# Kernel optimization log

Measured on AMD Instinct MI355X. Metric: run time of the kernel, lower is better.

## Reference

```python
import jax, jax.numpy as jnp
import numpy as np

N_NODES = 100000
N_EDGES = 1600000
IN_DIM = 128
HID_DIM = 128
OUT_DIM = 2


def sage_conv(x, src, dst, deg_inv, W_l, W_r, b):
    # mean-aggregate neighbor features: messages flow src -> dst
    agg = jax.ops.segment_sum(x[src], dst, num_segments=N_NODES)  # [N, d_in]
    agg = agg * deg_inv[:, None]
    # PyG SAGEConv: out = lin_l(aggr) + lin_r(x); bias only on lin_l
    return agg @ W_l + x @ W_r + b


def setup_inputs() -> dict:
    key = jax.random.key(0)
    ks = jax.random.split(key, 9)
    x = jax.random.normal(ks[0], (N_NODES, IN_DIM), dtype=jnp.float32)
    edge_index = jax.random.randint(ks[1], (2, N_EDGES), 0, N_NODES, dtype=jnp.int64)

    def glorot(k, shape):
        lim = float(np.sqrt(6.0 / (shape[0] + shape[1])))
        return jax.random.uniform(k, shape, jnp.float32, -lim, lim)

    return {
        "x": x,
        "edge_index": edge_index,
        "W1_l": glorot(ks[2], (IN_DIM, HID_DIM)),
        "W1_r": glorot(ks[3], (IN_DIM, HID_DIM)),
        "b1": jnp.zeros((HID_DIM,), jnp.float32),
        "W2_l": glorot(ks[4], (HID_DIM, HID_DIM)),
        "W2_r": glorot(ks[5], (HID_DIM, HID_DIM)),
        "b2": jnp.zeros((HID_DIM,), jnp.float32),
        "W3_l": glorot(ks[6], (HID_DIM, OUT_DIM)),
        "W3_r": glorot(ks[7], (HID_DIM, OUT_DIM)),
        "b3": jnp.zeros((OUT_DIM,), jnp.float32),
    }


def reference(x, edge_index, W1_l, W1_r, b1, W2_l, W2_r, b2, W3_l, W3_r, b3):
    src, dst = edge_index[0], edge_index[1]
    # mean-aggregation normalization: 1/in-degree (clamped to >=1)
    deg = jax.ops.segment_sum(jnp.ones((N_EDGES,), jnp.float32), dst, num_segments=N_NODES)
    deg_inv = 1.0 / jnp.maximum(deg, 1.0)

    h = sage_conv(x, src, dst, deg_inv, W1_l, W1_r, b1)
    h = jax.nn.relu(h)  # dropout is identity in eval mode
    h = sage_conv(h, src, dst, deg_inv, W2_l, W2_r, b2)
    h = jax.nn.relu(h)
    h = sage_conv(h, src, dst, deg_inv, W3_l, W3_r, b3)
    h = jax.nn.relu(h)
    return jax.nn.log_softmax(h, axis=1)
```

## Files before the change

kernel.cpp:

```cpp
#include <hip/hip_runtime.h>
#include <hip/hip_bf16.h>
#include <math.h>

#define DIM 128

typedef __attribute__((ext_vector_type(8))) short bf16x8;
typedef __attribute__((ext_vector_type(4))) float f32x4;

__device__ __forceinline__ ushort f2bf(float f) {
  unsigned u = __float_as_uint(f);
  return (ushort)((u + 0x7FFFu + ((u >> 16) & 1u)) >> 16);
}
__device__ __forceinline__ float bf2f(ushort h) {
  return __uint_as_float(((unsigned)h) << 16);
}

__global__ __launch_bounds__(256) void prep_kernel(
    const int* __restrict__ dst, unsigned* __restrict__ deg, unsigned* __restrict__ rank, int E,
    const float* __restrict__ x, ushort* __restrict__ xh, long total,
    const float* __restrict__ W1l, const float* __restrict__ W1r,
    const float* __restrict__ W2l, const float* __restrict__ W2r,
    ushort* __restrict__ tabs, int H, int C) {
  const int bid = blockIdx.x;
  const int r = bid % 3;
  const int q = bid / 3;
  if (r == 0) {
    if (q < H) {
      int gid = q * 256 + threadIdx.x;
      if (gid < E) rank[gid] = atomicAdd(&deg[dst[gid]], 1u);
    }
    return;
  }
  int id2 = q * 2 + (r - 1);
  if (id2 < C) {
    long i = ((long)id2 * 256 + threadIdx.x) * 4;
    if (i >= total) return;
    float4 v = *(const float4*)(x + i);
    uint2 Hh;
    Hh.x = (unsigned)f2bf(v.x) | ((unsigned)f2bf(v.y) << 16);
    Hh.y = (unsigned)f2bf(v.z) | ((unsigned)f2bf(v.w) << 16);
    *(uint2*)(xh + i) = Hh;
    return;
  }
  id2 -= C;
  if (id2 >= 256) return;
  int m = id2 >> 6;
  const float* W = (m == 0) ? W1l : (m == 1) ? W1r : (m == 2) ? W2l : W2r;
  ushort* Ht = tabs + (size_t)m * 16384;
  int idx = (id2 & 63) * 256 + threadIdx.x;
  int k = idx >> 7, n = idx & 127;
  Ht[n * DIM + k] = f2bf(W[idx]);
}

__global__ __launch_bounds__(256) void scan_block_kernel(const unsigned* __restrict__ deg,
                                                         unsigned* __restrict__ excl,
                                                         unsigned* __restrict__ partial,
                                                         float* __restrict__ dinv, int N) {
  __shared__ unsigned s[256];
  int i = blockIdx.x * 256 + threadIdx.x;
  unsigned v = (i < N) ? deg[i] : 0u;
  if (i < N) dinv[i] = 1.0f / fmaxf((float)v, 1.0f);
  s[threadIdx.x] = v;
  __syncthreads();
#pragma unroll
  for (int d = 1; d < 256; d <<= 1) {
    unsigned t = (threadIdx.x >= d) ? s[threadIdx.x - d] : 0u;
    __syncthreads();
    s[threadIdx.x] += t;
    __syncthreads();
  }
  if (i < N) excl[i] = s[threadIdx.x] - v;
  if (threadIdx.x == 255) partial[blockIdx.x] = s[255];
}

__global__ __launch_bounds__(256) void scan_partials_kernel(unsigned* __restrict__ partial, int B) {
  __shared__ unsigned s[256];
  __shared__ unsigned carry;
  if (threadIdx.x == 0) carry = 0u;
  __syncthreads();
  for (int base = 0; base < B; base += 256) {
    int i = base + threadIdx.x;
    unsigned v = (i < B) ? partial[i] : 0u;
    s[threadIdx.x] = v;
    __syncthreads();
#pragma unroll
    for (int d = 1; d < 256; d <<= 1) {
      unsigned t = (threadIdx.x >= d) ? s[threadIdx.x - d] : 0u;
      __syncthreads();
      s[threadIdx.x] += t;
      __syncthreads();
    }
    if (i < B) partial[i] = carry + s[threadIdx.x] - v;
    __syncthreads();
    if (threadIdx.x == 0) carry += s[255];
    __syncthreads();
  }
}

__global__ __launch_bounds__(256) void add_offsets_kernel(const unsigned* __restrict__ excl,
                                                          const unsigned* __restrict__ partial,
                                                          unsigned* __restrict__ off, int N, int E) {
  int i = blockIdx.x * 256 + threadIdx.x;
  if (i < N) off[i] = excl[i] + partial[i >> 8];
  if (i == N) off[N] = (unsigned)E;
}

__global__ __launch_bounds__(256) void csr_fill_kernel(const int* __restrict__ src,
                                                       const int* __restrict__ dst,
                                                       const unsigned* __restrict__ rank,
                                                       const unsigned* __restrict__ off,
                                                       int* __restrict__ csr_src, int E) {
  int e = blockIdx.x * 256 + threadIdx.x;
  if (e >= E) return;
  csr_src[off[dst[e]] + rank[e]] = src[e];
}

__global__ __launch_bounds__(256) void gather_wave_kernel(
    const ushort* __restrict__ featH, const int* __restrict__ csr_src,
    const unsigned* __restrict__ off, const float* __restrict__ dinv,
    ushort* __restrict__ aggH, int N) {
  const int node = (blockIdx.x * 256 + threadIdx.x) >> 6;
  if (node >= N) return;
  const int lane = threadIdx.x & 63;
  const int eslot = lane >> 4;
  const int col = lane & 15;
  const unsigned beg = off[node], end = off[node + 1];
  const ushort* fbase = featH + col * 8;

  float acc[8];
#pragma unroll
  for (int t = 0; t < 8; ++t) acc[t] = 0.f;

  auto accum = [&](int4 v) {
    unsigned w0 = (unsigned)v.x, w1 = (unsigned)v.y, w2 = (unsigned)v.z, w3 = (unsigned)v.w;
    acc[0] += __uint_as_float(w0 << 16);
    acc[1] += __uint_as_float(w0 & 0xFFFF0000u);
    acc[2] += __uint_as_float(w1 << 16);
    acc[3] += __uint_as_float(w1 & 0xFFFF0000u);
    acc[4] += __uint_as_float(w2 << 16);
    acc[5] += __uint_as_float(w2 & 0xFFFF0000u);
    acc[6] += __uint_as_float(w3 << 16);
    acc[7] += __uint_as_float(w3 & 0xFFFF0000u);
  };

  unsigned base = beg;
  for (; base + 16 <= end; base += 16) {
    int s0 = csr_src[base + eslot];
    int s1 = csr_src[base + 4 + eslot];
    int s2 = csr_src[base + 8 + eslot];
    int s3 = csr_src[base + 12 + eslot];
    int4 v0 = *(const int4*)(fbase + (size_t)s0 * DIM);
    int4 v1 = *(const int4*)(fbase + (size_t)s1 * DIM);
    int4 v2 = *(const int4*)(fbase + (size_t)s2 * DIM);
    int4 v3 = *(const int4*)(fbase + (size_t)s3 * DIM);
    accum(v0); accum(v1); accum(v2); accum(v3);
  }
  for (; base + 8 <= end; base += 8) {
    int s0 = csr_src[base + eslot];
    int s1 = csr_src[base + 4 + eslot];
    int4 v0 = *(const int4*)(fbase + (size_t)s0 * DIM);
    int4 v1 = *(const int4*)(fbase + (size_t)s1 * DIM);
    accum(v0); accum(v1);
  }
  for (unsigned e = base + eslot; e < end; e += 4) {
    int s = csr_src[e];
    int4 v = *(const int4*)(fbase + (size_t)s * DIM);
    accum(v);
  }

#pragma unroll
  for (int t = 0; t < 8; ++t) {
    acc[t] += __shfl_xor(acc[t], 32, 64);
    acc[t] += __shfl_xor(acc[t], 16, 64);
  }

  if (eslot == 0) {
    float di = dinv[node];
    unsigned ph[4];
#pragma unroll
    for (int t = 0; t < 4; ++t) {
      ph[t] = (unsigned)f2bf(acc[2 * t] * di) | ((unsigned)f2bf(acc[2 * t + 1] * di) << 16);
    }
    *(int4*)(aggH + (size_t)node * DIM + col * 8) =
        make_int4((int)ph[0], (int)ph[1], (int)ph[2], (int)ph[3]);
  }
}

__global__ __launch_bounds__(256) void sage_mfma_kernel(
    const ushort* __restrict__ aggH, const ushort* xH,
    const ushort* __restrict__ WlH, const ushort* __restrict__ WrH,
    const float* __restrict__ bias,
    const float* __restrict__ W3l, const float* __restrict__ W3r,
    ushort* __restrict__ outH, float* __restrict__ y, int N) {
  __shared__ ushort As[128 * 64];
  __shared__ ushort Bs[128 * 64];

  const int tid = threadIdx.x;
  const int bm = blockIdx.x * 128;
  const int wave = tid >> 6;
  const int lane = tid & 63;
  const int l15 = lane & 15;
  const int quad = lane >> 4;
  const int wm = wave >> 1;
  const int wn = wave & 1;

  f32x4 acc[4][4];
#pragma unroll
  for (int i = 0; i < 4; ++i)
#pragma unroll
    for (int j = 0; j < 4; ++j) acc[i][j] = (f32x4){0.f, 0.f, 0.f, 0.f};

  for (int g = 0; g < 4; ++g) {
    const ushort* Ap = (g < 2) ? aggH : xH;
    const ushort* Wp = (g < 2) ? WlH : WrH;
    const int kt = (g & 1) << 6;
    __syncthreads();
#pragma unroll
    for (int c = 0; c < 4; ++c) {
      int flat = c * 256 + tid;
      int row = flat >> 3;
      int kg = flat & 7;
      int swz = (kg ^ (row & 7)) << 3;
      int grow = bm + row;
      if (grow >= N) grow = N - 1;
      *(int4*)(&As[row * 64 + swz]) = *(const int4*)(Ap + (size_t)grow * DIM + kt + kg * 8);
      *(int4*)(&Bs[row * 64 + swz]) = *(const int4*)(Wp + (size_t)row * DIM + kt + kg * 8);
    }
    __syncthreads();
#pragma unroll
    for (int ks = 0; ks < 2; ++ks) {
      bf16x8 af[4], bfr[4];
      int kg = (ks << 2) + quad;
#pragma unroll
      for (int i = 0; i < 4; ++i) {
        int ar = (wm << 6) + (i << 4) + l15;
        af[i] = *(const bf16x8*)(&As[ar * 64 + ((kg ^ (ar & 7)) << 3)]);
        int br = (wn << 6) + (i << 4) + l15;
        bfr[i] = *(const bf16x8*)(&Bs[br * 64 + ((kg ^ (br & 7)) << 3)]);
      }
#pragma unroll
      for (int i = 0; i < 4; ++i)
#pragma unroll
        for (int j = 0; j < 4; ++j)
          acc[i][j] = __builtin_amdgcn_mfma_f32_16x16x32_bf16(af[i], bfr[j], acc[i][j], 0, 0, 0);
    }
  }

  __syncthreads();
  float* WcF = reinterpret_cast<float*>(As);
  float* YpF = reinterpret_cast<float*>(As) + 512;

  if (W3l) {
    for (int t = tid; t < 512; t += 256) {
      int col = t >> 2, c = t & 3;
      WcF[t] = (c < 2) ? W3l[col * 2 + c] : W3r[col * 2 + (c - 2)];
    }
    __syncthreads();
  }

  float bv[4];
#pragma unroll
  for (int j = 0; j < 4; ++j) bv[j] = bias[(wn << 6) + (j << 4) + l15];

#pragma unroll
  for (int i = 0; i < 4; ++i) {
#pragma unroll
    for (int r = 0; r < 4; ++r) {
      const int rowl = (wm << 6) + (i << 4) + (quad << 2) + r;
      const int grow = bm + rowl;
      float p0 = 0.f, p1 = 0.f, p2 = 0.f, p3 = 0.f;
#pragma unroll
      for (int j = 0; j < 4; ++j) {
        int col = (wn << 6) + (j << 4) + l15;
        float v = fmaxf(acc[i][j][r] + bv[j], 0.f);
        ushort h = f2bf(v);
        if (outH && grow < N) outH[(size_t)grow * DIM + col] = h;
        if (W3l) {
          float qv = bf2f(h);
          p0 += qv * WcF[col * 4 + 0];
          p1 += qv * WcF[col * 4 + 1];
          p2 += qv * WcF[col * 4 + 2];
          p3 += qv * WcF[col * 4 + 3];
        }
      }
      if (W3l) {
#pragma unroll
        for (int o = 1; o < 16; o <<= 1) {
          p0 += __shfl_xor(p0, o, 64);
          p1 += __shfl_xor(p1, o, 64);
          p2 += __shfl_xor(p2, o, 64);
          p3 += __shfl_xor(p3, o, 64);
        }
        if (l15 == 0) {
          YpF[(rowl * 4 + 0) * 2 + wn] = p0;
          YpF[(rowl * 4 + 1) * 2 + wn] = p1;
          YpF[(rowl * 4 + 2) * 2 + wn] = p2;
          YpF[(rowl * 4 + 3) * 2 + wn] = p3;
        }
      }
    }
  }

  if (W3l) {
    __syncthreads();
    for (int t = tid; t < 512; t += 256) {
      int grow = bm + (t >> 2);
      if (grow < N) y[(size_t)grow * 4 + (t & 3)] = YpF[t * 2 + 0] + YpF[t * 2 + 1];
    }
  }
}

__global__ __launch_bounds__(256) void final3_kernel(const float* __restrict__ y,
                                                     const int* __restrict__ csr_src,
                                                     const unsigned* __restrict__ off,
                                                     const float* __restrict__ dinv,
                                                     const float* __restrict__ b3,
                                                     float* __restrict__ out, int N) {
  int n = blockIdx.x * 256 + threadIdx.x;
  if (n >= N) return;
  unsigned beg = off[n], end = off[n + 1];
  float s0 = 0.f, s1 = 0.f;
  for (unsigned e = beg; e < end; ++e) {
    int s = csr_src[e];
    float2 v = *reinterpret_cast<const float2*>(&y[(size_t)s * 4]);
    s0 += v.x; s1 += v.y;
  }
  float di = dinv[n];
  float o0 = fmaxf(s0 * di + y[(size_t)n * 4 + 2] + b3[0], 0.f);
  float o1 = fmaxf(s1 * di + y[(size_t)n * 4 + 3] + b3[1], 0.f);
  float m = fmaxf(o0, o1);
  float l = m + logf(expf(o0 - m) + expf(o1 - m));
  out[n * 2 + 0] = o0 - l;
  out[n * 2 + 1] = o1 - l;
}

extern "C" void kernel_launch(void* const* d_in, const int* in_sizes, int n_in,
                              void* d_out, int out_size, void* d_ws, size_t ws_size,
                              hipStream_t stream) {
  const float* x   = (const float*)d_in[0];
  const int*   ei  = (const int*)d_in[1];
  const float* W1l = (const float*)d_in[2];
  const float* W1r = (const float*)d_in[3];
  const float* b1  = (const float*)d_in[4];
  const float* W2l = (const float*)d_in[5];
  const float* W2r = (const float*)d_in[6];
  const float* b2  = (const float*)d_in[7];
  const float* W3l = (const float*)d_in[8];
  const float* W3r = (const float*)d_in[9];
  const float* b3  = (const float*)d_in[10];

  const int N = in_sizes[0] / DIM;
  const int E = in_sizes[1] / 2;
  const int* src = ei;
  const int* dst = ei + E;
  const int B = (N + 255) / 256;

  char* ws = (char*)d_ws;
  size_t off_b = 0;
  auto alloc = [&](size_t bytes) {
    void* p = ws + off_b;
    off_b = (off_b + bytes + 255) & ~(size_t)255;
    return p;
  };
  unsigned* deg     = (unsigned*)alloc((size_t)N * 4);
  unsigned* excl    = (unsigned*)alloc((size_t)N * 4);
  unsigned* partial = (unsigned*)alloc((size_t)B * 4);
  unsigned* offs    = (unsigned*)alloc((size_t)(N + 1) * 4);
  unsigned* rank    = (unsigned*)alloc((size_t)E * 4);
  int*      csr_src = (int*)alloc((size_t)E * 4);
  float*    dinv    = (float*)alloc((size_t)N * 4);
  ushort*   xH      = (ushort*)alloc((size_t)N * DIM * 2);
  ushort*   aggH    = (ushort*)alloc((size_t)N * DIM * 2);
  ushort*   wtabs   = (ushort*)alloc((size_t)4 * 16384 * 2);
  float*    y       = (float*)alloc((size_t)N * 4 * 4);

  const int H = (E + 255) / 256;
  const int C = (int)(((size_t)N * DIM / 4 + 255) / 256);
  const int third = (H > (C + 257) / 2) ? H : (C + 257) / 2;
  hipMemsetAsync(deg, 0, (size_t)N * 4, stream);
  prep_kernel<<<third * 3, 256, 0, stream>>>(dst, deg, rank, E, x, xH, (long)N * DIM,
                                             W1l, W1r, W2l, W2r, wtabs, H, C);

  scan_block_kernel<<<B, 256, 0, stream>>>(deg, excl, partial, dinv, N);
  scan_partials_kernel<<<1, 256, 0, stream>>>(partial, B);
  add_offsets_kernel<<<(N + 256) / 256, 256, 0, stream>>>(excl, partial, offs, N, E);
  csr_fill_kernel<<<(E + 255) / 256, 256, 0, stream>>>(src, dst, rank, offs, csr_src, E);

  const ushort* W1lH = wtabs;
  const ushort* W1rH = wtabs + 16384;
  const ushort* W2lH = wtabs + 32768;
  const ushort* W2rH = wtabs + 49152;

  const int G = (N + 127) / 128;
  const int gather_grid = (N + 3) / 4;

  gather_wave_kernel<<<gather_grid, 256, 0, stream>>>(xH, csr_src, offs, dinv, aggH, N);
  sage_mfma_kernel<<<G, 256, 0, stream>>>(aggH, xH, W1lH, W1rH, b1,
                                          nullptr, nullptr, xH, nullptr, N);
  gather_wave_kernel<<<gather_grid, 256, 0, stream>>>(xH, csr_src, offs, dinv, aggH, N);
  sage_mfma_kernel<<<G, 256, 0, stream>>>(aggH, xH, W2lH, W2rH, b2,
                                          W3l, W3r, nullptr, y, N);
  final3_kernel<<<(N + 255) / 256, 256, 0, stream>>>(y, csr_src, offs, dinv, b3, (float*)d_out, N);
}
```

Before: 390.0 us.

## Transform features before aggregation and fuse GEMM epilogues into gather kernels

Reorders each SAGE layer to project first and aggregate afterwards, using the linearity of mean aggregation. Layer 1's x@W_l and x@W_r are computed by MFMA inside the prep kernel, overlapping with the degree atomics. Gather kernels then add the root term, bias and ReLU in their epilogue, and layer 3's projection also moves into the gather. This removes one full GEMM-over-aggregated-features pass and an intermediate write/read, at the cost of an extra N×128 bf16 buffer and different rounding (bf16 is rounded before aggregation rather than after).

```diff
diff --git a/kernel.cpp b/kernel.cpp
--- a/kernel.cpp
+++ b/kernel.cpp
@@ -1,5 +1,4 @@
 #include <hip/hip_runtime.h>
-#include <hip/hip_bf16.h>
 #include <math.h>
 
 #define DIM 128
@@ -15,41 +14,120 @@
   return __uint_as_float(((unsigned)h) << 16);
 }
 
-__global__ __launch_bounds__(256) void prep_kernel(
+__global__ __launch_bounds__(256) void prep2_kernel(
     const int* __restrict__ dst, unsigned* __restrict__ deg, unsigned* __restrict__ rank, int E,
-    const float* __restrict__ x, ushort* __restrict__ xh, long total,
+    const float* __restrict__ x,
     const float* __restrict__ W1l, const float* __restrict__ W1r,
+    ushort* __restrict__ xl, ushort* __restrict__ xr,
     const float* __restrict__ W2l, const float* __restrict__ W2r,
-    ushort* __restrict__ tabs, int H, int C) {
+    ushort* __restrict__ tabs, int H, int G1, int N) {
+  __shared__ ushort As[128 * 64];
+  __shared__ ushort Bs[128 * 64];
+  const int tid = threadIdx.x;
   const int bid = blockIdx.x;
-  const int r = bid % 3;
-  const int q = bid / 3;
-  if (r == 0) {
-    if (q < H) {
-      int gid = q * 256 + threadIdx.x;
+  const int r5 = bid % 5;
+  const int q5 = bid / 5;
+
+  if (r5 != 4) {
+    int hid = q5 * 4 + r5;
+    if (hid < H) {
+      int gid = hid * 256 + tid;
       if (gid < E) rank[gid] = atomicAdd(&deg[dst[gid]], 1u);
     }
     return;
   }
-  int id2 = q * 2 + (r - 1);
-  if (id2 < C) {
-    long i = ((long)id2 * 256 + threadIdx.x) * 4;
-    if (i >= total) return;
-    float4 v = *(const float4*)(x + i);
-    uint2 Hh;
-    Hh.x = (unsigned)f2bf(v.x) | ((unsigned)f2bf(v.y) << 16);
-    Hh.y = (unsigned)f2bf(v.z) | ((unsigned)f2bf(v.w) << 16);
-    *(uint2*)(xh + i) = Hh;
+  int aid = q5;
+  if (aid >= 2 * G1) {
+    int aid2 = aid - 2 * G1;
+    if (aid2 < 128) {
+      int m = aid2 >> 6;
+      const float* W = m ? W2r : W2l;
+      ushort* Ht = tabs + (size_t)m * 16384;
+      int idx = (aid2 & 63) * 256 + tid;
+      int k = idx >> 7, n = idx & 127;
+      Ht[n * DIM + k] = f2bf(W[idx]);
+    }
     return;
   }
-  id2 -= C;
-  if (id2 >= 256) return;
-  int m = id2 >> 6;
-  const float* W = (m == 0) ? W1l : (m == 1) ? W1r : (m == 2) ? W2l : W2r;
-  ushort* Ht = tabs + (size_t)m * 16384;
-  int idx = (id2 & 63) * 256 + threadIdx.x;
-  int k = idx >> 7, n = idx & 127;
-  Ht[n * DIM + k] = f2bf(W[idx]);
+
+  const int m = aid / G1;
+  const int tile = aid % G1;
+  const int bm = tile * 128;
+  const float* W = m ? W1r : W1l;
+  ushort* out = m ? xr : xl;
+
+  const int wave = tid >> 6;
+  const int lane = tid & 63;
+  const int l15 = lane & 15;
+  const int quad = lane >> 4;
+  const int wm = wave >> 1;
+  const int wn = wave & 1;
+
+  f32x4 acc[4][4];
+#pragma unroll
+  for (int i = 0; i < 4; ++i)
+#pragma unroll
+    for (int j = 0; j < 4; ++j) acc[i][j] = (f32x4){0.f, 0.f, 0.f, 0.f};
+
+  for (int g = 0; g < 2; ++g) {
+    const int kt = g << 6;
+    __syncthreads();
+#pragma unroll
+    for (int c = 0; c < 8; ++c) {
+      int flat = c * 256 + tid;
+      int row = flat >> 4;
+      int q4 = flat & 15;
+      int grow = bm + row;
+      if (grow >= N) grow = N - 1;
+      float4 v = *(const float4*)(x + (size_t)grow * DIM + kt + q4 * 4);
+      int kb = q4 >> 1, ki = (q4 & 1) << 2;
+      uint2 pk;
+      pk.x = (unsigned)f2bf(v.x) | ((unsigned)f2bf(v.y) << 16);
+      pk.y = (unsigned)f2bf(v.z) | ((unsigned)f2bf(v.w) << 16);
+      *(uint2*)(&As[row * 64 + ((kb ^ (row & 7)) << 3) + ki]) = pk;
+    }
+#pragma unroll
+    for (int c = 0; c < 32; ++c) {
+      int idx = c * 256 + tid;
+      int kk = idx >> 7, n = idx & 127;
+      Bs[n * 64 + (((kk >> 3) ^ (n & 7)) << 3) + (kk & 7)] =
+          f2bf(W[(size_t)(kt + kk) * DIM + n]);
+    }
+    __syncthreads();
+#pragma unroll
+    for (int ks = 0; ks < 2; ++ks) {
+      bf16x8 af[4], bfr[4];
+      int kg = (ks << 2) + quad;
+#pragma unroll
+      for (int i = 0; i < 4; ++i) {
+        int ar = (wm << 6) + (i << 4) + l15;
+        af[i] = *(const bf16x8*)(&As[ar * 64 + ((kg ^ (ar & 7)) << 3)]);
+        int br = (wn << 6) + (i << 4) + l15;
+        bfr[i] = *(const bf16x8*)(&Bs[br * 64 + ((kg ^ (br & 7)) << 3)]);
+      }
+#pragma unroll
+      for (int i = 0; i < 4; ++i)
+#pragma unroll
+        for (int j = 0; j < 4; ++j)
+          acc[i][j] = __builtin_amdgcn_mfma_f32_16x16x32_bf16(af[i], bfr[j], acc[i][j], 0, 0, 0);
+    }
+  }
+
+#pragma unroll
+  for (int i = 0; i < 4; ++i) {
+#pragma unroll
+    for (int r = 0; r < 4; ++r) {
+      const int rowl = (wm << 6) + (i << 4) + (quad << 2) + r;
+      const int grow = bm + rowl;
+      if (grow < N) {
+#pragma unroll
+        for (int j = 0; j < 4; ++j) {
+          int col = (wn << 6) + (j << 4) + l15;
+          out[(size_t)grow * DIM + col] = f2bf(acc[i][j][r]);
+        }
+      }
+    }
+  }
 }
 
 __global__ __launch_bounds__(256) void scan_block_kernel(const unsigned* __restrict__ deg,
@@ -115,88 +193,101 @@
   csr_src[off[dst[e]] + rank[e]] = src[e];
 }
 
-__global__ __launch_bounds__(256) void gather_wave_kernel(
-    const ushort* __restrict__ featH, const int* __restrict__ csr_src,
+#define GATHER_BODY(TABLE)                                                       \
+  const int node = (blockIdx.x * 256 + threadIdx.x) >> 6;                        \
+  if (node >= N) return;                                                         \
+  const int lane = threadIdx.x & 63;                                             \
+  const int eslot = lane >> 4;                                                   \
+  const int col = lane & 15;                                                     \
+  const unsigned beg = off[node], end = off[node + 1];                           \
+  const ushort* fbase = (TABLE) + col * 8;                                       \
+  float acc[8];                                                                  \
+  _Pragma("unroll") for (int t = 0; t < 8; ++t) acc[t] = 0.f;                    \
+  auto accum = [&](int4 v) {                                                     \
+    unsigned w0 = (unsigned)v.x, w1 = (unsigned)v.y;                             \
+    unsigned w2 = (unsigned)v.z, w3 = (unsigned)v.w;                             \
+    acc[0] += __uint_as_float(w0 << 16);                                         \
+    acc[1] += __uint_as_float(w0 & 0xFFFF0000u);                                 \
+    acc[2] += __uint_as_float(w1 << 16);                                         \
+    acc[3] += __uint_as_float(w1 & 0xFFFF0000u);                                 \
+    acc[4] += __uint_as_float(w2 << 16);                                         \
+    acc[5] += __uint_as_float(w2 & 0xFFFF0000u);                                 \
+    acc[6] += __uint_as_float(w3 << 16);                                         \
+    acc[7] += __uint_as_float(w3 & 0xFFFF0000u);                                 \
+  };                                                                             \
+  unsigned base = beg;                                                           \
+  for (; base + 16 <= end; base += 16) {                                         \
+    int s0 = csr_src[base + eslot];                                              \
+    int s1 = csr_src[base + 4 + eslot];                                          \
+    int s2 = csr_src[base + 8 + eslot];                                          \
+    int s3 = csr_src[base + 12 + eslot];                                         \
+    int4 v0 = *(const int4*)(fbase + (size_t)s0 * DIM);                          \
+    int4 v1 = *(const int4*)(fbase + (size_t)s1 * DIM);                          \
+    int4 v2 = *(const int4*)(fbase + (size_t)s2 * DIM);                          \
+    int4 v3 = *(const int4*)(fbase + (size_t)s3 * DIM);                          \
+    accum(v0); accum(v1); accum(v2); accum(v3);                                  \
+  }                                                                              \
+  for (; base + 8 <= end; base += 8) {                                           \
+    int s0 = csr_src[base + eslot];                                              \
+    int s1 = csr_src[base + 4 + eslot];                                          \
+    int4 v0 = *(const int4*)(fbase + (size_t)s0 * DIM);                          \
+    int4 v1 = *(const int4*)(fbase + (size_t)s1 * DIM);                          \
+    accum(v0); accum(v1);                                                        \
+  }                                                                              \
+  for (unsigned e = base + eslot; e < end; e += 4) {                             \
+    int s = csr_src[e];                                                          \
+    int4 v = *(const int4*)(fbase + (size_t)s * DIM);                            \
+    accum(v);                                                                    \
+  }                                                                              \
+  _Pragma("unroll") for (int t = 0; t < 8; ++t) {                                \
+    acc[t] += __shfl_xor(acc[t], 32, 64);                                        \
+    acc[t] += __shfl_xor(acc[t], 16, 64);                                        \
+  }
+
+__global__ __launch_bounds__(256) void gather1_kernel(
+    const ushort* __restrict__ xl, const int* __restrict__ csr_src,
     const unsigned* __restrict__ off, const float* __restrict__ dinv,
-    ushort* __restrict__ aggH, int N) {
-  const int node = (blockIdx.x * 256 + threadIdx.x) >> 6;
-  if (node >= N) return;
-  const int lane = threadIdx.x & 63;
-  const int eslot = lane >> 4;
-  const int col = lane & 15;
-  const unsigned beg = off[node], end = off[node + 1];
-  const ushort* fbase = featH + col * 8;
-
-  float acc[8];
-#pragma unroll
-  for (int t = 0; t < 8; ++t) acc[t] = 0.f;
-
-  auto accum = [&](int4 v) {
-    unsigned w0 = (unsigned)v.x, w1 = (unsigned)v.y, w2 = (unsigned)v.z, w3 = (unsigned)v.w;
-    acc[0] += __uint_as_float(w0 << 16);
-    acc[1] += __uint_as_float(w0 & 0xFFFF0000u);
-    acc[2] += __uint_as_float(w1 << 16);
-    acc[3] += __uint_as_float(w1 & 0xFFFF0000u);
-    acc[4] += __uint_as_float(w2 << 16);
-    acc[5] += __uint_as_float(w2 & 0xFFFF0000u);
-    acc[6] += __uint_as_float(w3 << 16);
-    acc[7] += __uint_as_float(w3 & 0xFFFF0000u);
-  };
-
-  unsigned base = beg;
-  for (; base + 16 <= end; base += 16) {
-    int s0 = csr_src[base + eslot];
-    int s1 = csr_src[base + 4 + eslot];
-    int s2 = csr_src[base + 8 + eslot];
-    int s3 = csr_src[base + 12 + eslot];
-    int4 v0 = *(const int4*)(fbase + (size_t)s0 * DIM);
-    int4 v1 = *(const int4*)(fbase + (size_t)s1 * DIM);
-    int4 v2 = *(const int4*)(fbase + (size_t)s2 * DIM);
-    int4 v3 = *(const int4*)(fbase + (size_t)s3 * DIM);
-    accum(v0); accum(v1); accum(v2); accum(v3);
-  }
-  for (; base + 8 <= end; base += 8) {
-    int s0 = csr_src[base + eslot];
-    int s1 = csr_src[base + 4 + eslot];
-    int4 v0 = *(const int4*)(fbase + (size_t)s0 * DIM);
-    int4 v1 = *(const int4*)(fbase + (size_t)s1 * DIM);
-    accum(v0); accum(v1);
-  }
-  for (unsigned e = base + eslot; e < end; e += 4) {
-    int s = csr_src[e];
-    int4 v = *(const int4*)(fbase + (size_t)s * DIM);
-    accum(v);
-  }
-
-#pragma unroll
-  for (int t = 0; t < 8; ++t) {
-    acc[t] += __shfl_xor(acc[t], 32, 64);
-    acc[t] += __shfl_xor(acc[t], 16, 64);
-  }
-
+    const ushort* __restrict__ xr, const float* __restrict__ b1,
+    ushort* __restrict__ h1, int N) {
+  GATHER_BODY(xl)
   if (eslot == 0) {
     float di = dinv[node];
+    int4 xv = *(const int4*)(xr + (size_t)node * DIM + col * 8);
+    float4 ba = *(const float4*)(b1 + col * 8);
+    float4 bb = *(const float4*)(b1 + col * 8 + 4);
+    unsigned w0 = (unsigned)xv.x, w1 = (unsigned)xv.y;
+    unsigned w2 = (unsigned)xv.z, w3 = (unsigned)xv.w;
+    float h[8];
+    h[0] = fmaxf(acc[0] * di + __uint_as_float(w0 << 16) + ba.x, 0.f);
+    h[1] = fmaxf(acc[1] * di + __uint_as_float(w0 & 0xFFFF0000u) + ba.y, 0.f);
+    h[2] = fmaxf(acc[2] * di + __uint_as_float(w1 << 16) + ba.z, 0.f);
+    h[3] = fmaxf(acc[3] * di + __uint_as_float(w1 & 0xFFFF0000u) + ba.w, 0.f);
+    h[4] = fmaxf(acc[4] * di + __uint_as_float(w2 << 16) + bb.x, 0.f);
+    h[5] = fmaxf(acc[5] * di + __uint_as_float(w2 & 0xFFFF0000u) + bb.y, 0.f);
+    h[6] = fmaxf(acc[6] * di + __uint_as_float(w3 << 16) + bb.z, 0.f);
+    h[7] = fmaxf(acc[7] * di + __uint_as_float(w3 & 0xFFFF0000u) + bb.w, 0.f);
     unsigned ph[4];
 #pragma unroll
-    for (int t = 0; t < 4; ++t) {
-      ph[t] = (unsigned)f2bf(acc[2 * t] * di) | ((unsigned)f2bf(acc[2 * t + 1] * di) << 16);
-    }
-    *(int4*)(aggH + (size_t)node * DIM + col * 8) =
+    for (int t = 0; t < 4; ++t)
+      ph[t] = (unsigned)f2bf(h[2 * t]) | ((unsigned)f2bf(h[2 * t + 1]) << 16);
+    *(int4*)(h1 + (size_t)node * DIM + col * 8) =
         make_int4((int)ph[0], (int)ph[1], (int)ph[2], (int)ph[3]);
   }
 }
 
-__global__ __launch_bounds__(256) void sage_mfma_kernel(
-    const ushort* __restrict__ aggH, const ushort* xH,
-    const ushort* __restrict__ WlH, const ushort* __restrict__ WrH,
-    const float* __restrict__ bias,
-    const float* __restrict__ W3l, const float* __restrict__ W3r,
-    ushort* __restrict__ outH, float* __restrict__ y, int N) {
+__global__ __launch_bounds__(256) void gemm2_kernel(
+    const ushort* __restrict__ h1, const ushort* __restrict__ tabs,
+    const float* __restrict__ b2, ushort* __restrict__ h1l, ushort* __restrict__ h1r,
+    int G1, int N) {
   __shared__ ushort As[128 * 64];
   __shared__ ushort Bs[128 * 64];
-
   const int tid = threadIdx.x;
-  const int bm = blockIdx.x * 128;
+  const int m = blockIdx.x / G1;
+  const int tile = blockIdx.x % G1;
+  const int bm = tile * 128;
+  const ushort* Wt = tabs + (size_t)m * 16384;
+  ushort* out = m ? h1r : h1l;
+
   const int wave = tid >> 6;
   const int lane = tid & 63;
   const int l15 = lane & 15;
@@ -210,10 +301,8 @@
 #pragma unroll
     for (int j = 0; j < 4; ++j) acc[i][j] = (f32x4){0.f, 0.f, 0.f, 0.f};
 
-  for (int g = 0; g < 4; ++g) {
-    const ushort* Ap = (g < 2) ? aggH : xH;
-    const ushort* Wp = (g < 2) ? WlH : WrH;
-    const int kt = (g & 1) << 6;
+  for (int g = 0; g < 2; ++g) {
+    const int kt = g << 6;
     __syncthreads();
 #pragma unroll
     for (int c = 0; c < 4; ++c) {
@@ -223,8 +312,8 @@
       int swz = (kg ^ (row & 7)) << 3;
       int grow = bm + row;
       if (grow >= N) grow = N - 1;
-      *(int4*)(&As[row * 64 + swz]) = *(const int4*)(Ap + (size_t)grow * DIM + kt + kg * 8);
-      *(int4*)(&Bs[row * 64 + swz]) = *(const int4*)(Wp + (size_t)row * DIM + kt + kg * 8);
+      *(int4*)(&As[row * 64 + swz]) = *(const int4*)(h1 + (size_t)grow * DIM + kt + kg * 8);
+      *(int4*)(&Bs[row * 64 + swz]) = *(const int4*)(Wt + (size_t)row * DIM + kt + kg * 8);
     }
     __syncthreads();
 #pragma unroll
@@ -246,21 +335,10 @@
     }
   }
 
-  __syncthreads();
-  float* WcF = reinterpret_cast<float*>(As);
-  float* YpF = reinterpret_cast<float*>(As) + 512;
-
-  if (W3l) {
-    for (int t = tid; t < 512; t += 256) {
-      int col = t >> 2, c = t & 3;
-      WcF[t] = (c < 2) ? W3l[col * 2 + c] : W3r[col * 2 + (c - 2)];
-    }
-    __syncthreads();
-  }
-
   float bv[4];
 #pragma unroll
-  for (int j = 0; j < 4; ++j) bv[j] = bias[(wn << 6) + (j << 4) + l15];
+  for (int j = 0; j < 4; ++j)
+    bv[j] = m ? b2[(wn << 6) + (j << 4) + l15] : 0.f;
 
 #pragma unroll
   for (int i = 0; i < 4; ++i) {
@@ -268,45 +346,56 @@
     for (int r = 0; r < 4; ++r) {
       const int rowl = (wm << 6) + (i << 4) + (quad << 2) + r;
       const int grow = bm + rowl;
-      float p0 = 0.f, p1 = 0.f, p2 = 0.f, p3 = 0.f;
-#pragma unroll
-      for (int j = 0; j < 4; ++j) {
-        int col = (wn << 6) + (j << 4) + l15;
-        float v = fmaxf(acc[i][j][r] + bv[j], 0.f);
-        ushort h = f2bf(v);
-        if (outH && grow < N) outH[(size_t)grow * DIM + col] = h;
-        if (W3l) {
-          float qv = bf2f(h);
-          p0 += qv * WcF[col * 4 + 0];
-          p1 += qv * WcF[col * 4 + 1];
-          p2 += qv * WcF[col * 4 + 2];
-          p3 += qv * WcF[col * 4 + 3];
+      if (grow < N) {
+#pragma unroll
+        for (int j = 0; j < 4; ++j) {
+          int col = (wn << 6) + (j << 4) + l15;
+          out[(size_t)grow * DIM + col] = f2bf(acc[i][j][r] + bv[j]);
         }
       }
-      if (W3l) {
-#pragma unroll
-        for (int o = 1; o < 16; o <<= 1) {
-          p0 += __shfl_xor(p0, o, 64);
-          p1 += __shfl_xor(p1, o, 64);
-          p2 += __shfl_xor(p2, o, 64);
-          p3 += __shfl_xor(p3, o, 64);
-        }
-        if (l15 == 0) {
-          YpF[(rowl * 4 + 0) * 2 + wn] = p0;
-          YpF[(rowl * 4 + 1) * 2 + wn] = p1;
-          YpF[(rowl * 4 + 2) * 2 + wn] = p2;
-          YpF[(rowl * 4 + 3) * 2 + wn] = p3;
-        }
-      }
-    }
-  }
-
-  if (W3l) {
-    __syncthreads();
-    for (int t = tid; t < 512; t += 256) {
-      int grow = bm + (t >> 2);
-      if (grow < N) y[(size_t)grow * 4 + (t & 3)] = YpF[t * 2 + 0] + YpF[t * 2 + 1];
-    }
+    }
+  }
+}
+
+__global__ __launch_bounds__(256) void gather2_kernel(
+    const ushort* __restrict__ h1l, const int* __restrict__ csr_src,
+    const unsigned* __restrict__ off, const float* __restrict__ dinv,
+    const ushort* __restrict__ h1r, const float* __restrict__ W3l,
+    const float* __restrict__ W3r, float* __restrict__ y, int N) {
+  GATHER_BODY(h1l)
+  if (eslot == 0) {
+    float di = dinv[node];
+    int4 xv = *(const int4*)(h1r + (size_t)node * DIM + col * 8);
+    unsigned w0 = (unsigned)xv.x, w1 = (unsigned)xv.y;
+    unsigned w2 = (unsigned)xv.z, w3 = (unsigned)xv.w;
+    float h[8];
+    h[0] = fmaxf(acc[0] * di + __uint_as_float(w0 << 16), 0.f);
+    h[1] = fmaxf(acc[1] * di + __uint_as_float(w0 & 0xFFFF0000u), 0.f);
+    h[2] = fmaxf(acc[2] * di + __uint_as_float(w1 << 16), 0.f);
+    h[3] = fmaxf(acc[3] * di + __uint_as_float(w1 & 0xFFFF0000u), 0.f);
+    h[4] = fmaxf(acc[4] * di + __uint_as_float(w2 << 16), 0.f);
+    h[5] = fmaxf(acc[5] * di + __uint_as_float(w2 & 0xFFFF0000u), 0.f);
+    h[6] = fmaxf(acc[6] * di + __uint_as_float(w3 << 16), 0.f);
+    h[7] = fmaxf(acc[7] * di + __uint_as_float(w3 & 0xFFFF0000u), 0.f);
+    const int d0 = col * 8;
+    float y0 = 0.f, y1 = 0.f, y2 = 0.f, y3 = 0.f;
+#pragma unroll
+    for (int t = 0; t < 8; t += 2) {
+      float4 wl = *(const float4*)(W3l + (size_t)(d0 + t) * 2);
+      float4 wr = *(const float4*)(W3r + (size_t)(d0 + t) * 2);
+      y0 += h[t] * wl.x + h[t + 1] * wl.z;
+      y1 += h[t] * wl.y + h[t + 1] * wl.w;
+      y2 += h[t] * wr.x + h[t + 1] * wr.z;
+      y3 += h[t] * wr.y + h[t + 1] * wr.w;
+    }
+#pragma unroll
+    for (int o = 1; o < 16; o <<= 1) {
+      y0 += __shfl_xor(y0, o, 64);
+      y1 += __shfl_xor(y1, o, 64);
+      y2 += __shfl_xor(y2, o, 64);
+      y3 += __shfl_xor(y3, o, 64);
+    }
+    if (lane == 0) *(float4*)(y + (size_t)node * 4) = make_float4(y0, y1, y2, y3);
   }
 }
 
@@ -369,36 +458,32 @@
   unsigned* rank    = (unsigned*)alloc((size_t)E * 4);
   int*      csr_src = (int*)alloc((size_t)E * 4);
   float*    dinv    = (float*)alloc((size_t)N * 4);
-  ushort*   xH      = (ushort*)alloc((size_t)N * DIM * 2);
-  ushort*   aggH    = (ushort*)alloc((size_t)N * DIM * 2);
-  ushort*   wtabs   = (ushort*)alloc((size_t)4 * 16384 * 2);
+  ushort*   xl      = (ushort*)alloc((size_t)N * DIM * 2);
+  ushort*   xr      = (ushort*)alloc((size_t)N * DIM * 2);
+  ushort*   h1      = (ushort*)alloc((size_t)N * DIM * 2);
+  ushort*   tabs    = (ushort*)alloc((size_t)2 * 16384 * 2);
   float*    y       = (float*)alloc((size_t)N * 4 * 4);
-
-  const int H = (E + 255) / 256;
-  const int C = (int)(((size_t)N * DIM / 4 + 255) / 256);
-  const int third = (H > (C + 257) / 2) ? H : (C + 257) / 2;
+  ushort* h1l = xl;
+  ushort* h1r = xr;
+
+  const int H  = (E + 255) / 256;
+  const int G1 = (N + 127) / 128;
+  const int AUX = 2 * G1 + 128;
+  const int HQ = (H + 3) / 4;
+  const int P = (AUX > HQ) ? AUX : HQ;
+
   hipMemsetAsync(deg, 0, (size_t)N * 4, stream);
-  prep_kernel<<<third * 3, 256, 0, stream>>>(dst, deg, rank, E, x, xH, (long)N * DIM,
-                                             W1l, W1r, W2l, W2r, wtabs, H, C);
+  prep2_kernel<<<5 * P, 256, 0, stream>>>(dst, deg, rank, E, x, W1l, W1r, xl, xr,
+                                          W2l, W2r, tabs, H, G1, N);
 
   scan_block_kernel<<<B, 256, 0, stream>>>(deg, excl, partial, dinv, N);
   scan_partials_kernel<<<1, 256, 0, stream>>>(partial, B);
   add_offsets_kernel<<<(N + 256) / 256, 256, 0, stream>>>(excl, partial, offs, N, E);
   csr_fill_kernel<<<(E + 255) / 256, 256, 0, stream>>>(src, dst, rank, offs, csr_src, E);
 
-  const ushort* W1lH = wtabs;
-  const ushort* W1rH = wtabs + 16384;
-  const ushort* W2lH = wtabs + 32768;
-  const ushort* W2rH = wtabs + 49152;
-
-  const int G = (N + 127) / 128;
   const int gather_grid = (N + 3) / 4;
-
-  gather_wave_kernel<<<gather_grid, 256, 0, stream>>>(xH, csr_src, offs, dinv, aggH, N);
-  sage_mfma_kernel<<<G, 256, 0, stream>>>(aggH, xH, W1lH, W1rH, b1,
-                                          nullptr, nullptr, xH, nullptr, N);
-  gather_wave_kernel<<<gather_grid, 256, 0, stream>>>(xH, csr_src, offs, dinv, aggH, N);
-  sage_mfma_kernel<<<G, 256, 0, stream>>>(aggH, xH, W2lH, W2rH, b2,
-                                          W3l, W3r, nullptr, y, N);
+  gather1_kernel<<<gather_grid, 256, 0, stream>>>(xl, csr_src, offs, dinv, xr, b1, h1, N);
+  gemm2_kernel<<<2 * G1, 256, 0, stream>>>(h1, tabs, b2, h1l, h1r, G1, N);
+  gather2_kernel<<<gather_grid, 256, 0, stream>>>(h1l, csr_src, offs, dinv, h1r, W3l, W3r, y, N);
   final3_kernel<<<(N + 255) / 256, 256, 0, stream>>>(y, csr_src, offs, dinv, b3, (float*)d_out, N);
 }
```

New measurement: 399.5 us. 1.02x slower.
